# Optimization experiments

Hardware: AMD Instinct MI355X
Metric: run time of the kernel (lower is better)

## Reference

```python
import jax, jax.numpy as jnp
import numpy as np

B, S, D_IN, D_H = 16, 4096, 512, 512

def setup_inputs() -> dict:
    key = jax.random.key(0)
    ks = jax.random.split(key, 8)
    inp = {
        "input": jax.random.normal(ks[0], (B, D_IN), dtype=jnp.float32),
        "context": jax.random.normal(ks[1], (B, S, D_IN), dtype=jnp.float32),
        "mask": jax.random.bernoulli(ks[2], 0.2, (B, S)),
        # parameters (torch nn.Linear layout: W [out,in], b [out])
        "W_in": jax.random.normal(ks[3], (D_H, D_IN), dtype=jnp.float32) / np.sqrt(D_IN),
        "b_in": jax.random.normal(ks[4], (D_H,), dtype=jnp.float32) * 0.01,
        "W_ctx": jax.random.normal(ks[5], (D_H, D_IN), dtype=jnp.float32) / np.sqrt(D_IN),
        "b_ctx": jax.random.normal(ks[6], (D_H,), dtype=jnp.float32) * 0.01,
        "v": jax.random.normal(ks[7], (D_H,), dtype=jnp.float32),
    }
    return inp


def reference(input, context, mask, W_in, b_in, W_ctx, b_ctx, v):
    # inp: [B, H] projected decoder state
    inp = input @ W_in.T + b_in
    # ctx: [B, S, H] projected context (this is what the torch code matmuls
    # with the softmax weights, i.e. hidden lives in hidden_dim space)
    ctx = context @ W_ctx.T + b_ctx
    # additive (Bahdanau) scores: v . tanh(inp + ctx) -> [B, S]
    scores = jnp.einsum("h,bsh->bs", v, jnp.tanh(inp[:, None, :] + ctx))
    # masked positions get -inf so they receive zero softmax weight
    scores = jnp.where(mask, -jnp.inf, scores)
    attn = jax.nn.softmax(scores, axis=-1)  # [B, S]
    # weighted sum of projected context: [B, H]
    hidden = jnp.einsum("bsh,bs->bh", ctx, attn)
    return hidden, attn
```

## Files before the change

### kernel.cpp

```cpp
#include <hip/hip_runtime.h>
#include <hip/hip_bf16.h>

#define B_  16
#define S_  4096
#define DIN 512
#define DH  512

typedef _Float16 f16x8 __attribute__((ext_vector_type(8)));
typedef float    f32x4 __attribute__((ext_vector_type(4)));


__device__ __forceinline__ float fast_tanh(float x) {
    float e = __expf(2.f * x);
    return 1.f - 2.f * __builtin_amdgcn_rcpf(e + 1.f);
}

__device__ __forceinline__ void gload_lds16(const void* g, void* l) {
    __builtin_amdgcn_global_load_lds(
        (const __attribute__((address_space(1))) void*)g,
        (__attribute__((address_space(3))) void*)l, 16, 0, 0);
}

__device__ __forceinline__ int mask_at(const void* mask, int isByte, int idx) {
    return isByte ? (int)((const unsigned char*)mask)[idx]
                  : ((const int*)mask)[idx];
}

__global__ void prep_kernel(const float* __restrict__ input,
                            const float* __restrict__ W_in,
                            const float* __restrict__ b_in,
                            const float* __restrict__ W_ctx,
                            const float* __restrict__ b_ctx,
                            const void*  __restrict__ mask,
                            _Float16* __restrict__ W16,
                            float* __restrict__ addv,
                            float* __restrict__ zeroRegion,
                            int* __restrict__ maskflag) {
    int blk = blockIdx.x;
    int tid = threadIdx.x;
    if (blk < 256) {
        int base = blk * 1024 + tid * 4;
        float4 wv = *(const float4*)(W_ctx + base);
        union { _Float16 f[4]; ushort4 u; } cv;
        cv.f[0] = (_Float16)wv.x; cv.f[1] = (_Float16)wv.y;
        cv.f[2] = (_Float16)wv.z; cv.f[3] = (_Float16)wv.w;
        *(ushort4*)(W16 + base) = cv.u;
    } else if (blk < 288) {
        int t = blk - 256;
        int b = t >> 1;
        int h = ((t & 1) << 8) + tid;
        __shared__ float inrow[DIN];
        inrow[tid]       = input[b * DIN + tid];
        inrow[tid + 256] = input[b * DIN + tid + 256];
        __syncthreads();
        const float* wr = W_in + (size_t)h * DIN;
        float acc = 0.f;
        for (int k = 0; k < DIN; k += 4) {
            float4 w4 = *(const float4*)(wr + k);
            acc += w4.x * inrow[k] + w4.y * inrow[k + 1]
                 + w4.z * inrow[k + 2] + w4.w * inrow[k + 3];
        }
        addv[b * DH + h] = acc + b_in[h] + b_ctx[h];
    } else if (blk == 288) {
        const uint4* m4 = (const uint4*)mask;
        unsigned int orw = 0;
#pragma unroll
        for (int it = 0; it < 16; ++it) {
            uint4 w = m4[it * 256 + tid];
            orw |= (w.x | w.y | w.z | w.w);
        }
        int found = ((orw & 0xFFFFFF00u) != 0) ? 1 : 0;
        __shared__ int f;
        if (tid == 0) f = 0;
        __syncthreads();
        if (found) atomicOr(&f, 1);
        __syncthreads();
        if (tid == 0) maskflag[0] = f;
    } else {
        int base = (blk - 289) * 4096;
#pragma unroll
        for (int it = 0; it < 16; ++it)
            zeroRegion[base + it * 256 + tid] = 0.f;
    }
}

__global__ __launch_bounds__(512, 4)
void score_kernel(const float* __restrict__ context,
                  const _Float16* __restrict__ W16,
                  const float* __restrict__ addv,
                  const float* __restrict__ v,
                  float* __restrict__ scores) {
    __shared__ float    As[2][4096];
    __shared__ _Float16 Bs[2][8192];

    const int tid  = threadIdx.x;
    const int wave = tid >> 6;
    const int lane = tid & 63;
    const int l15  = lane & 15;
    const int q    = lane >> 4;
    const int sg   = wave >> 1;
    const int ng   = wave & 1;

    const int b  = blockIdx.x >> 6;
    const int st = (blockIdx.x & 63) >> 1;
    const int nt = blockIdx.x & 1;
    const int s0 = st * 128;
    const int n0 = nt * 256;

    const float* ctxA = context + ((size_t)b * S_ + s0) * DIN;

#define STAGE(kc_, buf_)                                                       \
    {                                                                          \
        _Pragma("unroll")                                                      \
        for (int u = 0; u < 4; ++u) {                                          \
            int id = wave * 4 + u;                                             \
            if (id < 16) {                                                     \
                int jm = id >> 1, p = id & 1;                                  \
                const float* g = ctxA + (size_t)(jm * 16 + l15) * DIN +        \
                                 (kc_) * 32 + q * 8 + p * 4;                   \
                gload_lds16(g, &As[buf_][jm * 512 + p * 256]);                 \
            } else {                                                           \
                int jn = id - 16;                                              \
                const _Float16* g = W16 +                                      \
                    (size_t)(n0 + jn * 16 + l15) * DIN + (kc_) * 32 + q * 8;   \
                gload_lds16(g, &Bs[buf_][jn * 512]);                           \
            }                                                                  \
        }                                                                      \
    }

    f32x4 acc[2][8];
#pragma unroll
    for (int jm = 0; jm < 2; ++jm)
#pragma unroll
        for (int jn = 0; jn < 8; ++jn) acc[jm][jn] = (f32x4){0.f, 0.f, 0.f, 0.f};

    STAGE(0, 0);

    for (int kc = 0; kc < 16; ++kc) {
        __syncthreads();
        int buf = kc & 1;
        if (kc + 1 < 16) STAGE(kc + 1, (kc + 1) & 1);

        f16x8 afr[2];
#pragma unroll
        for (int jm = 0; jm < 2; ++jm) {
            int jma = sg * 2 + jm;
            float4 x0 = *(const float4*)&As[buf][jma * 512 + lane * 4];
            float4 x1 = *(const float4*)&As[buf][jma * 512 + 256 + lane * 4];
            f16x8 t;
            t[0] = (_Float16)x0.x; t[1] = (_Float16)x0.y;
            t[2] = (_Float16)x0.z; t[3] = (_Float16)x0.w;
            t[4] = (_Float16)x1.x; t[5] = (_Float16)x1.y;
            t[6] = (_Float16)x1.z; t[7] = (_Float16)x1.w;
            afr[jm] = t;
        }
#pragma unroll
        for (int jn = 0; jn < 8; ++jn) {
            int jna = ng * 8 + jn;
            f16x8 bf = *(const f16x8*)&Bs[buf][jna * 512 + q * 128 + l15 * 8];
            acc[0][jn] = __builtin_amdgcn_mfma_f32_16x16x32_f16(afr[0], bf, acc[0][jn], 0, 0, 0);
            acc[1][jn] = __builtin_amdgcn_mfma_f32_16x16x32_f16(afr[1], bf, acc[1][jn], 0, 0, 0);
        }
    }

    const float* avb = addv + b * DH;
    float rowsum[2][4] = {{0.f,0.f,0.f,0.f},{0.f,0.f,0.f,0.f}};
#pragma unroll
    for (int jn = 0; jn < 8; ++jn) {
        int n = n0 + (ng * 8 + jn) * 16 + l15;
        float av = avb[n];
        float vv = v[n];
#pragma unroll
        for (int jm = 0; jm < 2; ++jm)
#pragma unroll
            for (int r = 0; r < 4; ++r)
                rowsum[jm][r] += vv * fast_tanh(acc[jm][jn][r] + av);
    }
#pragma unroll
    for (int jm = 0; jm < 2; ++jm)
#pragma unroll
        for (int r = 0; r < 4; ++r) {
            float s = rowsum[jm][r];
            s += __shfl_xor(s, 1, 16);
            s += __shfl_xor(s, 2, 16);
            s += __shfl_xor(s, 4, 16);
            s += __shfl_xor(s, 8, 16);
            if (l15 == 0) {
                int srow = s0 + (sg * 2 + jm) * 16 + q * 4 + r;
                atomicAdd(&scores[b * S_ + srow], s);
            }
        }
}

__global__ __launch_bounds__(256)
void stats_kernel(const float* __restrict__ scores,
                  const void* __restrict__ mask,
                  const int* __restrict__ maskflag,
                  float* __restrict__ stats) {
    __shared__ float rbuf[8];
    int b = blockIdx.x, tid = threadIdx.x;
    int wv = tid >> 6, ln = tid & 63;
    int isByte = maskflag[0];
    const float* sr = scores + b * S_;

    float mx = -__builtin_inff();
    float vals[16];
#pragma unroll
    for (int it = 0; it < 16; ++it) {
        int s = it * 256 + tid;
        float x = mask_at(mask, isByte, b * S_ + s) ? -__builtin_inff() : sr[s];
        vals[it] = x;
        mx = fmaxf(mx, x);
    }
    for (int o = 1; o < 64; o <<= 1) mx = fmaxf(mx, __shfl_xor(mx, o, 64));
    if (ln == 0) rbuf[wv] = mx;
    __syncthreads();
    mx = fmaxf(fmaxf(rbuf[0], rbuf[1]), fmaxf(rbuf[2], rbuf[3]));

    float sum = 0.f;
#pragma unroll
    for (int it = 0; it < 16; ++it) sum += __expf(vals[it] - mx);
    for (int o = 1; o < 64; o <<= 1) sum += __shfl_xor(sum, o, 64);
    __syncthreads();
    if (ln == 0) rbuf[4 + wv] = sum;
    __syncthreads();
    if (tid == 0) {
        sum = rbuf[4] + rbuf[5] + rbuf[6] + rbuf[7];
        stats[b * 2]     = mx;
        stats[b * 2 + 1] = 1.f / sum;
    }
}

__global__ __launch_bounds__(256)
void attnwsum_kernel(const float* __restrict__ scores,
                     const float* __restrict__ context,
                     const void* __restrict__ mask,
                     const int* __restrict__ maskflag,
                     const float* __restrict__ stats,
                     float* __restrict__ attn,
                     float* __restrict__ wsum) {
    __shared__ int   selIdx[256];
    __shared__ float selW[256];
    __shared__ int   selCount;

    int b  = blockIdx.x >> 4;
    int c0 = (blockIdx.x & 15) * 256;
    int tid = threadIdx.x;
    int isByte = maskflag[0];
    float mx  = stats[b * 2];
    float inv = stats[b * 2 + 1];

    if (tid == 0) selCount = 0;
    __syncthreads();

    int s = c0 + tid;
    int idx = b * S_ + s;
    float sc = mask_at(mask, isByte, idx) ? -__builtin_inff() : scores[idx];
    float p = __expf(sc - mx) * inv;
    attn[idx] = p;
    if (p > 1e-9f) {
        int k = atomicAdd(&selCount, 1);
        selIdx[k] = s;
        selW[k]  = p;
    }
    __syncthreads();

    int cnt = selCount;
    if (cnt == 0) return;
    const float* cb = context + (size_t)b * S_ * DIN;
    float a00 = 0.f, a01 = 0.f, a10 = 0.f, a11 = 0.f;
    float a20 = 0.f, a21 = 0.f, a30 = 0.f, a31 = 0.f;
    int i = 0;
    for (; i + 4 <= cnt; i += 4) {
        const float* c0p = cb + (size_t)selIdx[i]     * DIN;
        const float* c1p = cb + (size_t)selIdx[i + 1] * DIN;
        const float* c2p = cb + (size_t)selIdx[i + 2] * DIN;
        const float* c3p = cb + (size_t)selIdx[i + 3] * DIN;
        float w0 = selW[i], w1 = selW[i + 1], w2 = selW[i + 2], w3 = selW[i + 3];
        a00 += w0 * c0p[tid]; a01 += w0 * c0p[tid + 256];
        a10 += w1 * c1p[tid]; a11 += w1 * c1p[tid + 256];
        a20 += w2 * c2p[tid]; a21 += w2 * c2p[tid + 256];
        a30 += w3 * c3p[tid]; a31 += w3 * c3p[tid + 256];
    }
    float acc0 = (a00 + a10) + (a20 + a30);
    float acc1 = (a01 + a11) + (a21 + a31);
    for (; i < cnt; ++i) {
        const float* cr = cb + (size_t)selIdx[i] * DIN;
        float w = selW[i];
        acc0 += w * cr[tid];
        acc1 += w * cr[tid + 256];
    }
    atomicAdd(&wsum[b * DIN + tid], acc0);
    atomicAdd(&wsum[b * DIN + tid + 256], acc1);
}

__global__ __launch_bounds__(256)
void hidden_kernel(const float* __restrict__ W_ctx,
                   const float* __restrict__ b_ctx,
                   const float* __restrict__ wsum,
                   float* __restrict__ hidden) {
    int b = blockIdx.x >> 1;
    int tid = threadIdx.x;
    int h = ((blockIdx.x & 1) << 8) + tid;
    __shared__ float wrow[DIN];
    wrow[tid]       = wsum[b * DIN + tid];
    wrow[tid + 256] = wsum[b * DIN + tid + 256];
    __syncthreads();
    const float* wr = W_ctx + (size_t)h * DIN;
    float acc = 0.f;
    for (int k = 0; k < DIN; k += 4) {
        float4 w4 = *(const float4*)(wr + k);
        acc += w4.x * wrow[k] + w4.y * wrow[k + 1]
             + w4.z * wrow[k + 2] + w4.w * wrow[k + 3];
    }
    hidden[b * DH + h] = acc + b_ctx[h];
}

extern "C" void kernel_launch(void* const* d_in, const int* in_sizes, int n_in,
                              void* d_out, int out_size, void* d_ws, size_t ws_size,
                              hipStream_t stream) {
    const float* input   = (const float*)d_in[0];
    const float* context = (const float*)d_in[1];
    const void*  mask    = d_in[2];
    const float* W_in    = (const float*)d_in[3];
    const float* b_in    = (const float*)d_in[4];
    const float* W_ctx   = (const float*)d_in[5];
    const float* b_ctx   = (const float*)d_in[6];
    const float* v       = (const float*)d_in[7];

    char* ws = (char*)d_ws;
    _Float16* W16   = (_Float16*)ws;
    float* addv     = (float*)(ws + 524288);
    float* scores   = (float*)(ws + 557056);
    float* wsum     = (float*)(ws + 819200);
    int*   maskflag = (int*)(ws + 851968);
    float* stats    = (float*)(ws + 852096);

    float* hidden = (float*)d_out;
    float* attn   = (float*)d_out + B_ * DH;

    prep_kernel<<<355, 256, 0, stream>>>(input, W_in, b_in, W_ctx, b_ctx, mask,
                                         W16, addv, scores , maskflag);
    score_kernel<<<1024, 512, 0, stream>>>(context, W16, addv, v, scores);
    stats_kernel<<<B_, 256, 0, stream>>>(scores, mask, maskflag, stats);
    attnwsum_kernel<<<B_ * 16, 256, 0, stream>>>(scores, context, mask, maskflag,
                                                 stats, attn, wsum);
    hidden_kernel<<<B_ * 2, 256, 0, stream>>>(W_ctx, b_ctx, wsum, hidden);
}
```

Baseline: 298.6 us.

## Restructure score GEMM to full-N per block and split small kernels wider

The score kernel now has each block cover 256 sequence rows across all 512 hidden columns. Context is converted to fp16 once into LDS, the B fragments are read directly from global fp16 weights, and row scores are reduced in LDS instead of with global atomics. Softmax stats are computed as per-chunk partials merged in the attn kernel, and the prep and hidden matvecs split K across 16 lanes with shuffle reduction to use more blocks. This drops redundant A loads and the score-zeroing atomics. In exchange, grid size for the main GEMM falls to 256 blocks and B is read straight from global or cache with no LDS reuse.

Measured after the change: 324.3 us. +8.6%, slower.

```diff
diff --git a/kernel.cpp b/kernel.cpp
--- a/kernel.cpp
+++ b/kernel.cpp
@@ -13,12 +13,6 @@
 __device__ __forceinline__ float fast_tanh(float x) {
     float e = __expf(2.f * x);
     return 1.f - 2.f * __builtin_amdgcn_rcpf(e + 1.f);
-}
-
-__device__ __forceinline__ void gload_lds16(const void* g, void* l) {
-    __builtin_amdgcn_global_load_lds(
-        (const __attribute__((address_space(1))) void*)g,
-        (__attribute__((address_space(3))) void*)l, 16, 0, 0);
 }
 
 __device__ __forceinline__ int mask_at(const void* mask, int isByte, int idx) {
@@ -34,7 +28,7 @@
                             const void*  __restrict__ mask,
                             _Float16* __restrict__ W16,
                             float* __restrict__ addv,
-                            float* __restrict__ zeroRegion,
+                            float* __restrict__ wsum,
                             int* __restrict__ maskflag) {
     int blk = blockIdx.x;
     int tid = threadIdx.x;
@@ -45,23 +39,28 @@
         cv.f[0] = (_Float16)wv.x; cv.f[1] = (_Float16)wv.y;
         cv.f[2] = (_Float16)wv.z; cv.f[3] = (_Float16)wv.w;
         *(ushort4*)(W16 + base) = cv.u;
-    } else if (blk < 288) {
+    } else if (blk < 768) {
         int t = blk - 256;
-        int b = t >> 1;
-        int h = ((t & 1) << 8) + tid;
+        int b  = t >> 5;
+        int h0 = (t & 31) * 16;
         __shared__ float inrow[DIN];
         inrow[tid]       = input[b * DIN + tid];
         inrow[tid + 256] = input[b * DIN + tid + 256];
         __syncthreads();
-        const float* wr = W_in + (size_t)h * DIN;
+        int h  = h0 + (tid >> 4);
+        int ks = (tid & 15) * 32;
+        const float* wr = W_in + (size_t)h * DIN + ks;
         float acc = 0.f;
-        for (int k = 0; k < DIN; k += 4) {
+#pragma unroll
+        for (int k = 0; k < 32; k += 4) {
             float4 w4 = *(const float4*)(wr + k);
-            acc += w4.x * inrow[k] + w4.y * inrow[k + 1]
-                 + w4.z * inrow[k + 2] + w4.w * inrow[k + 3];
+            acc += w4.x * inrow[ks + k] + w4.y * inrow[ks + k + 1]
+                 + w4.z * inrow[ks + k + 2] + w4.w * inrow[ks + k + 3];
         }
-        addv[b * DH + h] = acc + b_in[h] + b_ctx[h];
-    } else if (blk == 288) {
+#pragma unroll
+        for (int o = 1; o < 16; o <<= 1) acc += __shfl_xor(acc, o, 16);
+        if ((tid & 15) == 0) addv[b * DH + h] = acc + b_in[h] + b_ctx[h];
+    } else if (blk == 768) {
         const uint4* m4 = (const uint4*)mask;
         unsigned int orw = 0;
 #pragma unroll
@@ -77,157 +76,178 @@
         __syncthreads();
         if (tid == 0) maskflag[0] = f;
     } else {
-        int base = (blk - 289) * 4096;
-#pragma unroll
-        for (int it = 0; it < 16; ++it)
-            zeroRegion[base + it * 256 + tid] = 0.f;
-    }
-}
-
-__global__ __launch_bounds__(512, 4)
+#pragma unroll
+        for (int it = 0; it < 32; ++it)
+            wsum[it * 256 + tid] = 0.f;
+    }
+}
+
+__global__ __launch_bounds__(512, 2)
 void score_kernel(const float* __restrict__ context,
                   const _Float16* __restrict__ W16,
                   const float* __restrict__ addv,
                   const float* __restrict__ v,
                   float* __restrict__ scores) {
-    __shared__ float    As[2][4096];
-    __shared__ _Float16 Bs[2][8192];
+    __shared__ _Float16 Abuf[2][32768];
+    __shared__ float avS[DH];
+    __shared__ float vvS[DH];
+    __shared__ float scoreAcc[64];
 
     const int tid  = threadIdx.x;
     const int wave = tid >> 6;
     const int lane = tid & 63;
     const int l15  = lane & 15;
     const int q    = lane >> 4;
-    const int sg   = wave >> 1;
-    const int ng   = wave & 1;
-
-    const int b  = blockIdx.x >> 6;
-    const int st = (blockIdx.x & 63) >> 1;
-    const int nt = blockIdx.x & 1;
-    const int s0 = st * 128;
-    const int n0 = nt * 256;
-
-    const float* ctxA = context + ((size_t)b * S_ + s0) * DIN;
-
-#define STAGE(kc_, buf_)                                                       \
+    const int b     = blockIdx.x >> 4;
+    const int sbase = (blockIdx.x & 15) * 256;
+    const int n0w   = wave * 64;
+
+    if (tid < DH) { avS[tid] = addv[b * DH + tid]; vvS[tid] = v[tid]; }
+    avS[tid < DH ? tid : tid] = avS[tid < DH ? tid : tid];
+    {
+    }
+
+    const _Float16* bp[4];
+#pragma unroll
+    for (int jn = 0; jn < 4; ++jn)
+        bp[jn] = W16 + (size_t)(n0w + jn * 16 + l15) * DIN + q * 8;
+
+    float4 La[8], Lb[8];
+#define ISSUE_LOADS(si_)                                                       \
     {                                                                          \
         _Pragma("unroll")                                                      \
-        for (int u = 0; u < 4; ++u) {                                          \
-            int id = wave * 4 + u;                                             \
-            if (id < 16) {                                                     \
-                int jm = id >> 1, p = id & 1;                                  \
-                const float* g = ctxA + (size_t)(jm * 16 + l15) * DIN +        \
-                                 (kc_) * 32 + q * 8 + p * 4;                   \
-                gload_lds16(g, &As[buf_][jm * 512 + p * 256]);                 \
-            } else {                                                           \
-                int jn = id - 16;                                              \
-                const _Float16* g = W16 +                                      \
-                    (size_t)(n0 + jn * 16 + l15) * DIN + (kc_) * 32 + q * 8;   \
-                gload_lds16(g, &Bs[buf_][jn * 512]);                           \
-            }                                                                  \
+        for (int u = 0; u < 8; ++u) {                                          \
+            int s = wave * 8 + u;                                              \
+            int row_g = sbase + (si_) * 64 + ((s >> 4) << 4) + l15;            \
+            const float* g = context + ((size_t)b * S_ + row_g) * DIN +        \
+                             ((s & 15) << 5) + q * 8;                          \
+            La[u] = *(const float4*)g;                                         \
+            Lb[u] = *(const float4*)(g + 4);                                   \
         }                                                                      \
     }
-
-    f32x4 acc[2][8];
-#pragma unroll
-    for (int jm = 0; jm < 2; ++jm)
-#pragma unroll
-        for (int jn = 0; jn < 8; ++jn) acc[jm][jn] = (f32x4){0.f, 0.f, 0.f, 0.f};
-
-    STAGE(0, 0);
-
-    for (int kc = 0; kc < 16; ++kc) {
-        __syncthreads();
-        int buf = kc & 1;
-        if (kc + 1 < 16) STAGE(kc + 1, (kc + 1) & 1);
-
-        f16x8 afr[2];
-#pragma unroll
-        for (int jm = 0; jm < 2; ++jm) {
-            int jma = sg * 2 + jm;
-            float4 x0 = *(const float4*)&As[buf][jma * 512 + lane * 4];
-            float4 x1 = *(const float4*)&As[buf][jma * 512 + 256 + lane * 4];
-            f16x8 t;
-            t[0] = (_Float16)x0.x; t[1] = (_Float16)x0.y;
-            t[2] = (_Float16)x0.z; t[3] = (_Float16)x0.w;
-            t[4] = (_Float16)x1.x; t[5] = (_Float16)x1.y;
-            t[6] = (_Float16)x1.z; t[7] = (_Float16)x1.w;
-            afr[jm] = t;
+#define CVT_WRITE(buf_)                                                        \
+    {                                                                          \
+        _Pragma("unroll")                                                      \
+        for (int u = 0; u < 8; ++u) {                                          \
+            int s = wave * 8 + u;                                              \
+            f16x8 t;                                                           \
+            t[0] = (_Float16)La[u].x; t[1] = (_Float16)La[u].y;                \
+            t[2] = (_Float16)La[u].z; t[3] = (_Float16)La[u].w;                \
+            t[4] = (_Float16)Lb[u].x; t[5] = (_Float16)Lb[u].y;                \
+            t[6] = (_Float16)Lb[u].z; t[7] = (_Float16)Lb[u].w;                \
+            *(f16x8*)&Abuf[buf_][s * 512 + lane * 8] = t;                      \
+        }                                                                      \
+    }
+
+    ISSUE_LOADS(0);
+    CVT_WRITE(0);
+    __syncthreads();
+
+    for (int si = 0; si < 4; ++si) {
+        const int buf = si & 1;
+        if (si + 1 < 4) ISSUE_LOADS(si + 1);
+
+        f32x4 acc[4][4];
+#pragma unroll
+        for (int jm = 0; jm < 4; ++jm)
+#pragma unroll
+            for (int jn = 0; jn < 4; ++jn) acc[jm][jn] = (f32x4){0.f,0.f,0.f,0.f};
+
+        f16x8 afr[2][4], bfr[2][4];
+#pragma unroll
+        for (int jm = 0; jm < 4; ++jm)
+            afr[0][jm] = *(const f16x8*)&Abuf[buf][jm * 8192 + lane * 8];
+#pragma unroll
+        for (int jn = 0; jn < 4; ++jn)
+            bfr[0][jn] = *(const f16x8*)bp[jn];
+
+#pragma unroll
+        for (int kc = 0; kc < 16; ++kc) {
+            int cur = kc & 1, nxt = cur ^ 1;
+            if (kc < 15) {
+#pragma unroll
+                for (int jm = 0; jm < 4; ++jm)
+                    afr[nxt][jm] = *(const f16x8*)
+                        &Abuf[buf][jm * 8192 + (kc + 1) * 512 + lane * 8];
+#pragma unroll
+                for (int jn = 0; jn < 4; ++jn)
+                    bfr[nxt][jn] = *(const f16x8*)(bp[jn] + (kc + 1) * 32);
+            }
+#pragma unroll
+            for (int jm = 0; jm < 4; ++jm)
+#pragma unroll
+                for (int jn = 0; jn < 4; ++jn)
+                    acc[jm][jn] = __builtin_amdgcn_mfma_f32_16x16x32_f16(
+                        afr[cur][jm], bfr[cur][jn], acc[jm][jn], 0, 0, 0);
         }
-#pragma unroll
-        for (int jn = 0; jn < 8; ++jn) {
-            int jna = ng * 8 + jn;
-            f16x8 bf = *(const f16x8*)&Bs[buf][jna * 512 + q * 128 + l15 * 8];
-            acc[0][jn] = __builtin_amdgcn_mfma_f32_16x16x32_f16(afr[0], bf, acc[0][jn], 0, 0, 0);
-            acc[1][jn] = __builtin_amdgcn_mfma_f32_16x16x32_f16(afr[1], bf, acc[1][jn], 0, 0, 0);
-        }
-    }
-
-    const float* avb = addv + b * DH;
-    float rowsum[2][4] = {{0.f,0.f,0.f,0.f},{0.f,0.f,0.f,0.f}};
-#pragma unroll
-    for (int jn = 0; jn < 8; ++jn) {
-        int n = n0 + (ng * 8 + jn) * 16 + l15;
-        float av = avb[n];
-        float vv = v[n];
-#pragma unroll
-        for (int jm = 0; jm < 2; ++jm)
-#pragma unroll
-            for (int r = 0; r < 4; ++r)
-                rowsum[jm][r] += vv * fast_tanh(acc[jm][jn][r] + av);
-    }
-#pragma unroll
-    for (int jm = 0; jm < 2; ++jm)
-#pragma unroll
-        for (int r = 0; r < 4; ++r) {
-            float s = rowsum[jm][r];
-            s += __shfl_xor(s, 1, 16);
-            s += __shfl_xor(s, 2, 16);
-            s += __shfl_xor(s, 4, 16);
-            s += __shfl_xor(s, 8, 16);
-            if (l15 == 0) {
-                int srow = s0 + (sg * 2 + jm) * 16 + q * 4 + r;
-                atomicAdd(&scores[b * S_ + srow], s);
+
+        if (si + 1 < 4) CVT_WRITE(buf ^ 1);
+
+        if (tid < 64) scoreAcc[tid] = 0.f;
+        __syncthreads();
+#pragma unroll
+        for (int jm = 0; jm < 4; ++jm) {
+            float rs[4] = {0.f, 0.f, 0.f, 0.f};
+#pragma unroll
+            for (int jn = 0; jn < 4; ++jn) {
+                int n = n0w + jn * 16 + l15;
+                float av = avS[n];
+                float vv = vvS[n];
+#pragma unroll
+                for (int r = 0; r < 4; ++r)
+                    rs[r] += vv * fast_tanh(acc[jm][jn][r] + av);
+            }
+#pragma unroll
+            for (int r = 0; r < 4; ++r) {
+                float s = rs[r];
+                s += __shfl_xor(s, 1, 16);
+                s += __shfl_xor(s, 2, 16);
+                s += __shfl_xor(s, 4, 16);
+                s += __shfl_xor(s, 8, 16);
+                if (l15 == 0)
+                    atomicAdd(&scoreAcc[jm * 16 + q * 4 + r], s);
             }
         }
+        __syncthreads();
+        if (tid < 64)
+            scores[b * S_ + sbase + si * 64 + tid] = scoreAcc[tid];
+        __syncthreads();
+    }
+#undef ISSUE_LOADS
+#undef CVT_WRITE
 }
 
 __global__ __launch_bounds__(256)
-void stats_kernel(const float* __restrict__ scores,
-                  const void* __restrict__ mask,
-                  const int* __restrict__ maskflag,
-                  float* __restrict__ stats) {
-    __shared__ float rbuf[8];
-    int b = blockIdx.x, tid = threadIdx.x;
+void statsP_kernel(const float* __restrict__ scores,
+                   const void* __restrict__ mask,
+                   const int* __restrict__ maskflag,
+                   float2* __restrict__ partials) {
+    __shared__ float rbuf[4];
+    int b  = blockIdx.x >> 4;
+    int c0 = (blockIdx.x & 15) * 256;
+    int tid = threadIdx.x;
     int wv = tid >> 6, ln = tid & 63;
     int isByte = maskflag[0];
-    const float* sr = scores + b * S_;
-
-    float mx = -__builtin_inff();
-    float vals[16];
-#pragma unroll
-    for (int it = 0; it < 16; ++it) {
-        int s = it * 256 + tid;
-        float x = mask_at(mask, isByte, b * S_ + s) ? -__builtin_inff() : sr[s];
-        vals[it] = x;
-        mx = fmaxf(mx, x);
-    }
+
+    int idx = b * S_ + c0 + tid;
+    float val = mask_at(mask, isByte, idx) ? -__builtin_inff() : scores[idx];
+
+    float mx = val;
     for (int o = 1; o < 64; o <<= 1) mx = fmaxf(mx, __shfl_xor(mx, o, 64));
     if (ln == 0) rbuf[wv] = mx;
     __syncthreads();
     mx = fmaxf(fmaxf(rbuf[0], rbuf[1]), fmaxf(rbuf[2], rbuf[3]));
-
-    float sum = 0.f;
-#pragma unroll
-    for (int it = 0; it < 16; ++it) sum += __expf(vals[it] - mx);
+    __syncthreads();
+
+    float e = __expf(val - mx);
+    if (val == -__builtin_inff()) e = 0.f;
+    float sum = e;
     for (int o = 1; o < 64; o <<= 1) sum += __shfl_xor(sum, o, 64);
-    __syncthreads();
-    if (ln == 0) rbuf[4 + wv] = sum;
+    if (ln == 0) rbuf[wv] = sum;
     __syncthreads();
     if (tid == 0) {
-        sum = rbuf[4] + rbuf[5] + rbuf[6] + rbuf[7];
-        stats[b * 2]     = mx;
-        stats[b * 2 + 1] = 1.f / sum;
+        sum = rbuf[0] + rbuf[1] + rbuf[2] + rbuf[3];
+        partials[blockIdx.x] = make_float2(mx, sum);
     }
 }
 
@@ -236,9 +256,10 @@
                      const float* __restrict__ context,
                      const void* __restrict__ mask,
                      const int* __restrict__ maskflag,
-                     const float* __restrict__ stats,
+                     const float2* __restrict__ partials,
                      float* __restrict__ attn,
                      float* __restrict__ wsum) {
+    __shared__ float pmx[16], psm[16];
     __shared__ int   selIdx[256];
     __shared__ float selW[256];
     __shared__ int   selCount;
@@ -247,11 +268,21 @@
     int c0 = (blockIdx.x & 15) * 256;
     int tid = threadIdx.x;
     int isByte = maskflag[0];
-    float mx  = stats[b * 2];
-    float inv = stats[b * 2 + 1];
-
+
+    if (tid < 16) {
+        float2 pp = partials[b * 16 + tid];
+        pmx[tid] = pp.x; psm[tid] = pp.y;
+    }
     if (tid == 0) selCount = 0;
     __syncthreads();
+    float mx = -__builtin_inff();
+#pragma unroll
+    for (int i = 0; i < 16; ++i) mx = fmaxf(mx, pmx[i]);
+    float sum = 0.f;
+#pragma unroll
+    for (int i = 0; i < 16; ++i)
+        if (psm[i] > 0.f) sum += psm[i] * __expf(pmx[i] - mx);
+    float inv = 1.f / sum;
 
     int s = c0 + tid;
     int idx = b * S_ + s;
@@ -299,21 +330,27 @@
                    const float* __restrict__ b_ctx,
                    const float* __restrict__ wsum,
                    float* __restrict__ hidden) {
-    int b = blockIdx.x >> 1;
+    int blk = blockIdx.x;
+    int b  = blk >> 5;
+    int h0 = (blk & 31) * 16;
     int tid = threadIdx.x;
-    int h = ((blockIdx.x & 1) << 8) + tid;
     __shared__ float wrow[DIN];
     wrow[tid]       = wsum[b * DIN + tid];
     wrow[tid + 256] = wsum[b * DIN + tid + 256];
     __syncthreads();
-    const float* wr = W_ctx + (size_t)h * DIN;
+    int h  = h0 + (tid >> 4);
+    int ks = (tid & 15) * 32;
+    const float* wr = W_ctx + (size_t)h * DIN + ks;
     float acc = 0.f;
-    for (int k = 0; k < DIN; k += 4) {
+#pragma unroll
+    for (int k = 0; k < 32; k += 4) {
         float4 w4 = *(const float4*)(wr + k);
-        acc += w4.x * wrow[k] + w4.y * wrow[k + 1]
-             + w4.z * wrow[k + 2] + w4.w * wrow[k + 3];
-    }
-    hidden[b * DH + h] = acc + b_ctx[h];
+        acc += w4.x * wrow[ks + k] + w4.y * wrow[ks + k + 1]
+             + w4.z * wrow[ks + k + 2] + w4.w * wrow[ks + k + 3];
+    }
+#pragma unroll
+    for (int o = 1; o < 16; o <<= 1) acc += __shfl_xor(acc, o, 16);
+    if ((tid & 15) == 0) hidden[b * DH + h] = acc + b_ctx[h];
 }
 
 extern "C" void kernel_launch(void* const* d_in, const int* in_sizes, int n_in,
@@ -334,16 +371,16 @@
     float* scores   = (float*)(ws + 557056);
     float* wsum     = (float*)(ws + 819200);
     int*   maskflag = (int*)(ws + 851968);
-    float* stats    = (float*)(ws + 852096);
+    float2* partials = (float2*)(ws + 852224);
 
     float* hidden = (float*)d_out;
     float* attn   = (float*)d_out + B_ * DH;
 
-    prep_kernel<<<355, 256, 0, stream>>>(input, W_in, b_in, W_ctx, b_ctx, mask,
-                                         W16, addv, scores , maskflag);
-    score_kernel<<<1024, 512, 0, stream>>>(context, W16, addv, v, scores);
-    stats_kernel<<<B_, 256, 0, stream>>>(scores, mask, maskflag, stats);
-    attnwsum_kernel<<<B_ * 16, 256, 0, stream>>>(scores, context, mask, maskflag,
-                                                 stats, attn, wsum);
-    hidden_kernel<<<B_ * 2, 256, 0, stream>>>(W_ctx, b_ctx, wsum, hidden);
-}
+    prep_kernel<<<770, 256, 0, stream>>>(input, W_in, b_in, W_ctx, b_ctx, mask,
+                                         W16, addv, wsum, maskflag);
+    score_kernel<<<256, 512, 0, stream>>>(context, W16, addv, v, scores);
+    statsP_kernel<<<256, 256, 0, stream>>>(scores, mask, maskflag, partials);
+    attnwsum_kernel<<<256, 256, 0, stream>>>(scores, context, mask, maskflag,
+                                             partials, attn, wsum);
+    hidden_kernel<<<512, 256, 0, stream>>>(W_ctx, b_ctx, wsum, hidden);
+}
```
